# Performance work log

Measured on AMD Instinct MI355X. Metric: run time of the kernel, lower is better.

The kernel has to match this reference:

```python
import jax, jax.numpy as jnp
import numpy as np

N_NODES = 50000
N_EDGES = 800000
D_FEAT = 96
OUT_DIM = 96


def setup_inputs() -> dict:
    key = jax.random.key(0)
    k1, k2, k3, k4 = jax.random.split(key, 4)
    x = jax.random.normal(k1, (N_NODES, D_FEAT), dtype=jnp.float32)
    W = jax.random.normal(k2, (D_FEAT, OUT_DIM), dtype=jnp.float32) / np.sqrt(D_FEAT)
    b = jnp.zeros((OUT_DIM,), dtype=jnp.float32)
    src = jax.random.randint(k3, (N_EDGES,), 0, N_NODES, dtype=jnp.int64)
    dst = jax.random.randint(k4, (N_EDGES,), 0, N_NODES, dtype=jnp.int64)
    return {"x": x, "W": W, "b": b, "src": src, "dst": dst}


def reference(x, W, b, src, dst):
    # GCNConv: symmetric degree normalization, transform-then-aggregate.
    ones = jnp.ones(src.shape[0], dtype=x.dtype)
    deg_out = jax.ops.segment_sum(ones, src, num_segments=N_NODES)  # [N]
    deg_in = jax.ops.segment_sum(ones, dst, num_segments=N_NODES)   # [N]
    inv_sqrt_out = jnp.where(deg_out > 0, jax.lax.rsqrt(deg_out), 0.0)
    inv_sqrt_in = jnp.where(deg_in > 0, jax.lax.rsqrt(deg_in), 0.0)

    h = x @ W  # [N, out_dim] - transform first (cheap GEMM)
    coef = inv_sqrt_out[src] * inv_sqrt_in[dst]         # [E]
    msg = h[src] * coef[:, None]                         # [E, out_dim] gather
    agg = jax.ops.segment_sum(msg, dst, num_segments=N_NODES)  # scatter-reduce
    return agg + b
```

## Files before the change

### kernel.cpp

```cpp
#include <hip/hip_runtime.h>

#define N_NODES 50000
#define N_EDGES 800000
#define DFEAT 96

#define RBITS  14
#define RSIZE  16384
#define NRANGE 4
#define NCHUNK 64
#define CHUNK_E (N_EDGES / NCHUNK)
#define HF_BLOCKS (NRANGE * NCHUNK)
#define NB 196

typedef short bf16x8 __attribute__((ext_vector_type(8)));
typedef float f32x4  __attribute__((ext_vector_type(4)));

__device__ __forceinline__ unsigned bpack(float a, float b) {
    unsigned ua = __float_as_uint(a);
    unsigned ub = __float_as_uint(b);
    ua = (ua + 0x7FFFu + ((ua >> 16) & 1u)) >> 16;
    ub = (ub + 0x7FFFu + ((ub >> 16) & 1u)) >> 16;
    return ua | (ub << 16);
}
__device__ __forceinline__ unsigned short b1(float a) {
    unsigned u = __float_as_uint(a);
    u = (u + 0x7FFFu + ((u >> 16) & 1u)) >> 16;
    return (unsigned short)u;
}

__global__ __launch_bounds__(512) void deg_hist_kernel(
    const int* __restrict__ src, const int* __restrict__ dst,
    unsigned* __restrict__ ptab) {
    __shared__ unsigned hh[RSIZE];
    int tid = threadIdx.x;
    int r = blockIdx.x & (NRANGE - 1);
    int c = blockIdx.x >> 2;
    for (int i = tid; i < RSIZE; i += 512) hh[i] = 0;
    __syncthreads();
    int lo = r << RBITS;
    const int4* s4 = (const int4*)(src + c * CHUNK_E);
    const int4* d4 = (const int4*)(dst + c * CHUNK_E);
    for (int i = tid; i < CHUNK_E / 4; i += 512) {
        int4 s = s4[i];
        int4 d = d4[i];
        unsigned a;
        a = (unsigned)(s.x - lo); if (a < RSIZE) atomicAdd(&hh[a], 1u);
        a = (unsigned)(s.y - lo); if (a < RSIZE) atomicAdd(&hh[a], 1u);
        a = (unsigned)(s.z - lo); if (a < RSIZE) atomicAdd(&hh[a], 1u);
        a = (unsigned)(s.w - lo); if (a < RSIZE) atomicAdd(&hh[a], 1u);
        a = (unsigned)(d.x - lo); if (a < RSIZE) atomicAdd(&hh[a], 0x10000u);
        a = (unsigned)(d.y - lo); if (a < RSIZE) atomicAdd(&hh[a], 0x10000u);
        a = (unsigned)(d.z - lo); if (a < RSIZE) atomicAdd(&hh[a], 0x10000u);
        a = (unsigned)(d.w - lo); if (a < RSIZE) atomicAdd(&hh[a], 0x10000u);
    }
    __syncthreads();
    unsigned* pt = ptab + ((size_t)blockIdx.x << RBITS);
    for (int i = tid; i < RSIZE; i += 512) pt[i] = hh[i];
}

__global__ __launch_bounds__(256) void deg_reduce_kernel(
    const unsigned* __restrict__ ptab, unsigned short* __restrict__ pfx,
    int* __restrict__ deg_out, int* __restrict__ deg_in,
    int* __restrict__ bsum) {
    __shared__ int ws[4];
    int tid = threadIdx.x;
    int n = blockIdx.x * 256 + tid;
    int so = 0, si = 0;
    if (n < N_NODES) {
        int r = n >> RBITS, bin = n & (RSIZE - 1);
        #pragma unroll 8
        for (int c = 0; c < NCHUNK; ++c) {
            size_t idx = (((size_t)(c * NRANGE + r)) << RBITS) + bin;
            unsigned v = ptab[idx];
            so += (int)(v & 0xffffu);
            pfx[idx] = (unsigned short)si;
            si += (int)(v >> 16);
        }
        deg_out[n] = so;
        deg_in[n]  = si;
    }
    int v = si;
    #pragma unroll
    for (int off = 32; off; off >>= 1) v += __shfl_down(v, off, 64);
    if ((tid & 63) == 0) ws[tid >> 6] = v;
    __syncthreads();
    if (tid == 0) bsum[blockIdx.x] = ws[0] + ws[1] + ws[2] + ws[3];
}

__global__ __launch_bounds__(256) void scan_final_kernel(
    const int* __restrict__ deg, const int* __restrict__ bsum,
    int* __restrict__ offs, int nb) {
    __shared__ int wsum[4];
    __shared__ int sbase;
    int tid = threadIdx.x, lane = tid & 63, wave = tid >> 6;
    int i = blockIdx.x * 256 + tid;
    int v = (i < N_NODES) ? deg[i] : 0;
    int x = v;
    #pragma unroll
    for (int off = 1; off < 64; off <<= 1) {
        int t = __shfl_up(x, off, 64);
        if (lane >= off) x += t;
    }
    if (lane == 63) wsum[wave] = x;
    if (wave == 0) {
        int s = 0;
        for (int j = lane; j < blockIdx.x; j += 64) s += bsum[j];
        #pragma unroll
        for (int off = 32; off; off >>= 1) s += __shfl_down(s, off, 64);
        if (lane == 0) sbase = s;
    }
    if (blockIdx.x == gridDim.x - 1 && wave == 1) {
        int s = 0;
        for (int j = lane; j < nb; j += 64) s += bsum[j];
        #pragma unroll
        for (int off = 32; off; off >>= 1) s += __shfl_down(s, off, 64);
        if (lane == 0) offs[N_NODES] = s;
    }
    __syncthreads();
    int wb = sbase;
    for (int w = 0; w < wave; ++w) wb += wsum[w];
    if (i < N_NODES) offs[i] = wb + x - v;
}

__global__ __launch_bounds__(512) void fill_kernel(
    const int* __restrict__ src, const int* __restrict__ dst,
    const int* __restrict__ offs, const unsigned short* __restrict__ pfx,
    int* __restrict__ csr_src) {
    __shared__ int cur[RSIZE];
    int tid = threadIdx.x;
    int r = blockIdx.x & (NRANGE - 1);
    int c = blockIdx.x >> 2;
    int lo = r << RBITS;
    const unsigned short* pf = pfx + ((size_t)blockIdx.x << RBITS);
    for (int i = tid; i < RSIZE; i += 512) {
        int gi = lo + i;
        int o = (gi < N_NODES) ? offs[gi] : 0;
        cur[i] = o + (int)pf[i];
    }
    __syncthreads();
    const int4* s4 = (const int4*)(src + c * CHUNK_E);
    const int4* d4 = (const int4*)(dst + c * CHUNK_E);
    for (int i = tid; i < CHUNK_E / 4; i += 512) {
        int4 s = s4[i];
        int4 d = d4[i];
        unsigned a;
        a = (unsigned)(d.x - lo); if (a < RSIZE) csr_src[atomicAdd(&cur[a], 1)] = s.x;
        a = (unsigned)(d.y - lo); if (a < RSIZE) csr_src[atomicAdd(&cur[a], 1)] = s.y;
        a = (unsigned)(d.z - lo); if (a < RSIZE) csr_src[atomicAdd(&cur[a], 1)] = s.z;
        a = (unsigned)(d.w - lo); if (a < RSIZE) csr_src[atomicAdd(&cur[a], 1)] = s.w;
    }
}

#define GEMM_ROWS 64
#define TLD 104
__global__ __launch_bounds__(256) void gemm_kernel(
    const float* __restrict__ x, const float* __restrict__ W,
    const int* __restrict__ deg_out, unsigned short* __restrict__ h, int nrows) {
    __shared__ unsigned short WT[96 * TLD];
    __shared__ unsigned short xA[GEMM_ROWS * TLD];
    int tid = threadIdx.x;
    int r0 = blockIdx.x * GEMM_ROWS;

    for (int i = tid; i < 48 * 96; i += 256) {
        int k2 = i / 96, n = i - k2 * 96;
        float w0 = W[(size_t)(2 * k2) * 96 + n];
        float w1 = W[(size_t)(2 * k2 + 1) * 96 + n];
        *(unsigned*)&WT[n * TLD + 2 * k2] = bpack(w0, w1);
    }
    for (int i = tid; i < GEMM_ROWS * 48; i += 256) {
        int m = i / 48, k2 = i - m * 48;
        int row = r0 + m; if (row >= nrows) row = nrows - 1;
        float2 v = *(const float2*)&x[(size_t)row * 96 + 2 * k2];
        *(unsigned*)&xA[m * TLD + 2 * k2] = bpack(v.x, v.y);
    }
    __syncthreads();

    int lane = tid & 63, wave = tid >> 6;
    int m16 = lane & 15;
    int g = lane >> 4;
    int rbase = wave * 16;

    bf16x8 afrag[3];
    #pragma unroll
    for (int ks = 0; ks < 3; ++ks)
        afrag[ks] = *(const bf16x8*)&xA[(rbase + m16) * TLD + ks * 32 + g * 8];

    f32x4 acc[6];
    #pragma unroll
    for (int nt = 0; nt < 6; ++nt) {
        f32x4 c = {0.f, 0.f, 0.f, 0.f};
        #pragma unroll
        for (int ks = 0; ks < 3; ++ks) {
            bf16x8 bfrag = *(const bf16x8*)&WT[(nt * 16 + m16) * TLD + ks * 32 + g * 8];
            c = __builtin_amdgcn_mfma_f32_16x16x32_bf16(afrag[ks], bfrag, c, 0, 0, 0);
        }
        acc[nt] = c;
    }

    float s[4];
    #pragma unroll
    for (int r = 0; r < 4; ++r) {
        int row = r0 + rbase + g * 4 + r;
        int d = (row < nrows) ? deg_out[row] : 1;
        s[r] = (d > 0) ? rsqrtf((float)d) : 0.f;
    }
    #pragma unroll
    for (int nt = 0; nt < 6; ++nt) {
        #pragma unroll
        for (int r = 0; r < 4; ++r) {
            int row = r0 + rbase + g * 4 + r;
            if (row < nrows)
                h[(size_t)row * 96 + nt * 16 + m16] = b1(acc[nt][r] * s[r]);
        }
    }
}

__device__ __forceinline__ void upadd(float* a, uint4 q) {
    a[0] += __uint_as_float(q.x << 16);
    a[1] += __uint_as_float(q.x & 0xffff0000u);
    a[2] += __uint_as_float(q.y << 16);
    a[3] += __uint_as_float(q.y & 0xffff0000u);
    a[4] += __uint_as_float(q.z << 16);
    a[5] += __uint_as_float(q.z & 0xffff0000u);
    a[6] += __uint_as_float(q.w << 16);
    a[7] += __uint_as_float(q.w & 0xffff0000u);
}

#define AGG_NODES 16
#define IDX_CAP 2048
__global__ __launch_bounds__(256) void agg_kernel(
    const unsigned short* __restrict__ h, const int* __restrict__ csr_src,
    const int* __restrict__ offs, const float* __restrict__ b,
    float* __restrict__ out) {
    __shared__ int sh_idx[IDX_CAP];
    __shared__ int sh_off[AGG_NODES + 1];
    int tid = threadIdx.x;
    int n0 = blockIdx.x * AGG_NODES;
    if (tid <= AGG_NODES) sh_off[tid] = offs[n0 + tid];
    __syncthreads();
    int s0 = sh_off[0];
    int len = sh_off[AGG_NODES] - s0;
    bool lds_ok = (len <= IDX_CAP);
    if (lds_ok) {
        for (int i = tid; i < len; i += 256) sh_idx[i] = csr_src[s0 + i];
    }
    __syncthreads();

    int node = tid >> 4;
    int lane16 = tid & 15;
    int j = lane16 & 3;
    int q = lane16 >> 2;
    int start = sh_off[node], end = sh_off[node + 1];
    float acc[24];
    #pragma unroll
    for (int i = 0; i < 24; ++i) acc[i] = 0.f;
    const uint4* hb = (const uint4*)h;

    int e = start + q;
    for (; e + 4 < end; e += 8) {
        int i0 = lds_ok ? sh_idx[e - s0] : csr_src[e];
        int i1 = lds_ok ? sh_idx[e + 4 - s0] : csr_src[e + 4];
        size_t b0 = (size_t)i0 * 12 + j;
        size_t b1 = (size_t)i1 * 12 + j;
        uint4 q0 = hb[b0], q1 = hb[b0 + 4], q2 = hb[b0 + 8];
        uint4 p0 = hb[b1], p1 = hb[b1 + 4], p2 = hb[b1 + 8];
        upadd(acc + 0, q0); upadd(acc + 8, q1); upadd(acc + 16, q2);
        upadd(acc + 0, p0); upadd(acc + 8, p1); upadd(acc + 16, p2);
    }
    if (e < end) {
        int i0 = lds_ok ? sh_idx[e - s0] : csr_src[e];
        size_t b0 = (size_t)i0 * 12 + j;
        uint4 q0 = hb[b0], q1 = hb[b0 + 4], q2 = hb[b0 + 8];
        upadd(acc + 0, q0); upadd(acc + 8, q1); upadd(acc + 16, q2);
    }
    #pragma unroll
    for (int i = 0; i < 24; ++i) {
        acc[i] += __shfl_xor(acc[i], 4, 64);
        acc[i] += __shfl_xor(acc[i], 8, 64);
    }
    if (q != 0) return;
    float inv = (end > start) ? rsqrtf((float)(end - start)) : 0.f;
    int n = n0 + node;
    #pragma unroll
    for (int g = 0; g < 3; ++g) {
        int slot = j + 4 * g;
        float4 bb0 = *(const float4*)(b + 8 * slot);
        float4 bb1 = *(const float4*)(b + 8 * slot + 4);
        float4 r0, r1;
        r0.x = acc[g * 8 + 0] * inv + bb0.x;
        r0.y = acc[g * 8 + 1] * inv + bb0.y;
        r0.z = acc[g * 8 + 2] * inv + bb0.z;
        r0.w = acc[g * 8 + 3] * inv + bb0.w;
        r1.x = acc[g * 8 + 4] * inv + bb1.x;
        r1.y = acc[g * 8 + 5] * inv + bb1.y;
        r1.z = acc[g * 8 + 6] * inv + bb1.z;
        r1.w = acc[g * 8 + 7] * inv + bb1.w;
        float4* o = (float4*)(out + (size_t)n * DFEAT + 8 * slot);
        o[0] = r0; o[1] = r1;
    }
}

extern "C" void kernel_launch(void* const* d_in, const int* in_sizes, int n_in,
                              void* d_out, int out_size, void* d_ws, size_t ws_size,
                              hipStream_t stream) {
    const float* x  = (const float*)d_in[0];
    const float* W  = (const float*)d_in[1];
    const float* b  = (const float*)d_in[2];
    const int*   src = (const int*)d_in[3];
    const int*   dst = (const int*)d_in[4];
    float* out = (float*)d_out;

    int* deg_out = (int*)d_ws;
    int* deg_in  = deg_out + N_NODES;
    int* offs    = deg_in + N_NODES;
    int* csr_src = offs + N_NODES + 1;
    int* bsum    = csr_src + N_EDGES;
    size_t off1 = (((size_t)(3 * N_NODES + 1 + N_EDGES + 256)) * 4 + 255) & ~(size_t)255;
    unsigned* ptab = (unsigned*)((char*)d_ws + off1);
    size_t off2 = off1 + ((size_t)HF_BLOCKS << RBITS) * 4;
    unsigned short* pfx = (unsigned short*)((char*)d_ws + off2);
    size_t off3 = (off2 + ((size_t)HF_BLOCKS << RBITS) * 2 + 255) & ~(size_t)255;
    unsigned short* h = (unsigned short*)((char*)d_ws + off3);

    deg_hist_kernel<<<HF_BLOCKS, 512, 0, stream>>>(src, dst, ptab);
    deg_reduce_kernel<<<NB, 256, 0, stream>>>(ptab, pfx, deg_out, deg_in, bsum);
    scan_final_kernel<<<NB, 256, 0, stream>>>(deg_in, bsum, offs, NB);
    fill_kernel<<<HF_BLOCKS, 512, 0, stream>>>(src, dst, offs, pfx, csr_src);
    gemm_kernel<<<(N_NODES + GEMM_ROWS - 1) / GEMM_ROWS, 256, 0, stream>>>(
        x, W, deg_out, h, N_NODES);
    agg_kernel<<<N_NODES / AGG_NODES, 256, 0, stream>>>(h, csr_src, offs, b, out);
}
```

Measured before the change: 148.1 us.

## Split h into column planes and aggregate each plane in a separate pass

The GEMM now writes h as three column-planar slabs of 32 bf16 columns each, and the aggregation kernel is launched three times, once per slab, accumulating 8 columns per thread. This shrinks the random-gather working set per pass so it fits better in cache. The cost is reading the CSR index and offset arrays three times, two extra kernel launches, and smaller 64-byte gather segments per edge.

Measured after the change: 157.7 us. +6.5%, slower.

```diff
diff --git a/kernel.cpp b/kernel.cpp
--- a/kernel.cpp
+++ b/kernel.cpp
@@ -206,16 +206,18 @@
     }
     #pragma unroll
     for (int nt = 0; nt < 6; ++nt) {
+        int col = nt * 16 + m16;
+        int part = col >> 5, pc = col & 31;
         #pragma unroll
         for (int r = 0; r < 4; ++r) {
             int row = r0 + rbase + g * 4 + r;
             if (row < nrows)
-                h[(size_t)row * 96 + nt * 16 + m16] = b1(acc[nt][r] * s[r]);
+                h[((size_t)part * N_NODES + row) * 32 + pc] = b1(acc[nt][r] * s[r]);
         }
     }
 }
 
-__device__ __forceinline__ void upadd(float* a, uint4 q) {
+__device__ __forceinline__ void upadd8(float* a, uint4 q) {
     a[0] += __uint_as_float(q.x << 16);
     a[1] += __uint_as_float(q.x & 0xffff0000u);
     a[2] += __uint_as_float(q.y << 16);
@@ -231,7 +233,7 @@
 __global__ __launch_bounds__(256) void agg_kernel(
     const unsigned short* __restrict__ h, const int* __restrict__ csr_src,
     const int* __restrict__ offs, const float* __restrict__ b,
-    float* __restrict__ out) {
+    float* __restrict__ out, int part) {
     __shared__ int sh_idx[IDX_CAP];
     __shared__ int sh_off[AGG_NODES + 1];
     int tid = threadIdx.x;
@@ -251,53 +253,47 @@
     int j = lane16 & 3;
     int q = lane16 >> 2;
     int start = sh_off[node], end = sh_off[node + 1];
-    float acc[24];
-    #pragma unroll
-    for (int i = 0; i < 24; ++i) acc[i] = 0.f;
-    const uint4* hb = (const uint4*)h;
+    float acc[8];
+    #pragma unroll
+    for (int i = 0; i < 8; ++i) acc[i] = 0.f;
+    const uint4* hb = (const uint4*)(h + (size_t)part * N_NODES * 32);
 
     int e = start + q;
     for (; e + 4 < end; e += 8) {
         int i0 = lds_ok ? sh_idx[e - s0] : csr_src[e];
         int i1 = lds_ok ? sh_idx[e + 4 - s0] : csr_src[e + 4];
-        size_t b0 = (size_t)i0 * 12 + j;
-        size_t b1 = (size_t)i1 * 12 + j;
-        uint4 q0 = hb[b0], q1 = hb[b0 + 4], q2 = hb[b0 + 8];
-        uint4 p0 = hb[b1], p1 = hb[b1 + 4], p2 = hb[b1 + 8];
-        upadd(acc + 0, q0); upadd(acc + 8, q1); upadd(acc + 16, q2);
-        upadd(acc + 0, p0); upadd(acc + 8, p1); upadd(acc + 16, p2);
+        uint4 q0 = hb[(size_t)i0 * 4 + j];
+        uint4 p0 = hb[(size_t)i1 * 4 + j];
+        upadd8(acc, q0);
+        upadd8(acc, p0);
     }
     if (e < end) {
         int i0 = lds_ok ? sh_idx[e - s0] : csr_src[e];
-        size_t b0 = (size_t)i0 * 12 + j;
-        uint4 q0 = hb[b0], q1 = hb[b0 + 4], q2 = hb[b0 + 8];
-        upadd(acc + 0, q0); upadd(acc + 8, q1); upadd(acc + 16, q2);
-    }
-    #pragma unroll
-    for (int i = 0; i < 24; ++i) {
+        uint4 q0 = hb[(size_t)i0 * 4 + j];
+        upadd8(acc, q0);
+    }
+    #pragma unroll
+    for (int i = 0; i < 8; ++i) {
         acc[i] += __shfl_xor(acc[i], 4, 64);
         acc[i] += __shfl_xor(acc[i], 8, 64);
     }
     if (q != 0) return;
     float inv = (end > start) ? rsqrtf((float)(end - start)) : 0.f;
     int n = n0 + node;
-    #pragma unroll
-    for (int g = 0; g < 3; ++g) {
-        int slot = j + 4 * g;
-        float4 bb0 = *(const float4*)(b + 8 * slot);
-        float4 bb1 = *(const float4*)(b + 8 * slot + 4);
-        float4 r0, r1;
-        r0.x = acc[g * 8 + 0] * inv + bb0.x;
-        r0.y = acc[g * 8 + 1] * inv + bb0.y;
-        r0.z = acc[g * 8 + 2] * inv + bb0.z;
-        r0.w = acc[g * 8 + 3] * inv + bb0.w;
-        r1.x = acc[g * 8 + 4] * inv + bb1.x;
-        r1.y = acc[g * 8 + 5] * inv + bb1.y;
-        r1.z = acc[g * 8 + 6] * inv + bb1.z;
-        r1.w = acc[g * 8 + 7] * inv + bb1.w;
-        float4* o = (float4*)(out + (size_t)n * DFEAT + 8 * slot);
-        o[0] = r0; o[1] = r1;
-    }
+    int colbase = part * 32 + j * 8;
+    float4 bb0 = *(const float4*)(b + colbase);
+    float4 bb1 = *(const float4*)(b + colbase + 4);
+    float4 r0, r1;
+    r0.x = acc[0] * inv + bb0.x;
+    r0.y = acc[1] * inv + bb0.y;
+    r0.z = acc[2] * inv + bb0.z;
+    r0.w = acc[3] * inv + bb0.w;
+    r1.x = acc[4] * inv + bb1.x;
+    r1.y = acc[5] * inv + bb1.y;
+    r1.z = acc[6] * inv + bb1.z;
+    r1.w = acc[7] * inv + bb1.w;
+    float4* o = (float4*)(out + (size_t)n * DFEAT + colbase);
+    o[0] = r0; o[1] = r1;
 }
 
 extern "C" void kernel_launch(void* const* d_in, const int* in_sizes, int n_in,
@@ -328,5 +324,6 @@
     fill_kernel<<<HF_BLOCKS, 512, 0, stream>>>(src, dst, offs, pfx, csr_src);
     gemm_kernel<<<(N_NODES + GEMM_ROWS - 1) / GEMM_ROWS, 256, 0, stream>>>(
         x, W, deg_out, h, N_NODES);
-    agg_kernel<<<N_NODES / AGG_NODES, 256, 0, stream>>>(h, csr_src, offs, b, out);
-}
+    for (int p = 0; p < 3; ++p)
+        agg_kernel<<<N_NODES / AGG_NODES, 256, 0, stream>>>(h, csr_src, offs, b, out, p);
+}
```
